# Kernel tuning notes

Measured on AMD Instinct MI355X. Metric: run time of the kernel, lower is better.

Reference implementation:

```python
import jax, jax.numpy as jnp
import numpy as np

N = 100000
E = 1600000
D = 128          # f_gru_in == f_gru_out
G = 128          # f_gather
K = 4            # n_etypes
STEPS = 3        # n_gconv_steps


def setup_inputs() -> dict:
    key = jax.random.key(0)
    ks = jax.random.split(key, 16)
    s = 0.05
    return {
        "features": jax.random.normal(ks[0], (N, D), jnp.float32),
        "src": jax.random.randint(ks[1], (E,), 0, N, jnp.int32),
        "dst": jax.random.randint(ks[2], (E,), 0, N, jnp.int32),
        "etypes": jax.random.randint(ks[3], (E,), 0, K, jnp.int32),
        # per-etype edge linears (torch Linear: y = x W^T + b)
        "W_et": jax.random.normal(ks[4], (K, D, D), jnp.float32) * s,
        "b_et": jax.random.normal(ks[5], (K, D), jnp.float32) * s,
        # GRUCell weights, torch gate order (r, z, n)
        "W_ih": jax.random.normal(ks[6], (3 * D, D), jnp.float32) * s,
        "b_ih": jax.random.normal(ks[7], (3 * D,), jnp.float32) * s,
        "W_hh": jax.random.normal(ks[8], (3 * D, D), jnp.float32) * s,
        "b_hh": jax.random.normal(ks[9], (3 * D,), jnp.float32) * s,
        # gated output head
        "i_w": jax.random.normal(ks[10], (G, D + D), jnp.float32) * s,
        "i_b": jax.random.normal(ks[11], (G,), jnp.float32) * s,
        "j_w": jax.random.normal(ks[12], (G, D), jnp.float32) * s,
        "j_b": jax.random.normal(ks[13], (G,), jnp.float32) * s,
    }


def _gru_cell(a, h, W_ih, b_ih, W_hh, b_hh):
    gi = a @ W_ih.T + b_ih          # [N, 3D]
    gh = h @ W_hh.T + b_hh          # [N, 3D]
    ir, iz, in_ = jnp.split(gi, 3, axis=1)
    hr, hz, hn = jnp.split(gh, 3, axis=1)
    r = jax.nn.sigmoid(ir + hr)
    z = jax.nn.sigmoid(iz + hz)
    n = jnp.tanh(in_ + r * hn)
    return (1.0 - z) * n + z * h


def reference(features, src, dst, etypes, W_et, b_et, W_ih, b_ih, W_hh, b_hh,
              i_w, i_b, j_w, j_b):
    n_nodes = features.shape[0]
    h = features  # in_feats == out_feats -> no zero padding needed
    for _ in range(STEPS):
        # transform all nodes by every etype linear: [K, N, D]
        t = jnp.einsum('nd,kod->kno', h, W_et) + b_et[:, None, :]
        # gather per-edge message by (etype, src) then scatter-add to dst
        msg = t[etypes, src]                                  # [E, D]
        a = jax.ops.segment_sum(msg, dst, num_segments=n_nodes)
        h = _gru_cell(a, h, W_ih, b_ih, W_hh, b_hh)
    # dropout p=0 (eval) -> identity; gated output head
    gate = jax.nn.sigmoid(jnp.concatenate([h, features], axis=1) @ i_w.T + i_b)
    return gate * (h @ j_w.T + j_b)
```

## Files before the change

### kernel.cpp

```cpp
#include <hip/hip_runtime.h>
#include <hip/hip_bf16.h>

typedef __bf16 bf16;
typedef __attribute__((ext_vector_type(8))) __bf16 bf16x8;
typedef __attribute__((ext_vector_type(4))) float f32x4;

union BP { unsigned u; bf16 b[2]; };

#define SB() __builtin_amdgcn_sched_barrier(0)

__device__ __forceinline__ void dma16(const void* g, void* l) {
  __builtin_amdgcn_global_load_lds(
      (const __attribute__((address_space(1))) unsigned*)g,
      (__attribute__((address_space(3))) unsigned*)l, 16, 0, 0);
}

__global__ __launch_bounds__(256) void fused_k(const bf16* __restrict__ big,
                                               bf16* __restrict__ hbp,
                                               const bf16* __restrict__ wb,
                                               int M)
{
  const int lane = threadIdx.x & 63;
  const int w    = threadIdx.x >> 6;
  const int quad = lane >> 4;
  const int lr   = lane & 15;
  const int mbase = blockIdx.x * 128 + w * 32;

  __shared__ __align__(16) bf16 lds[128 * 136];
  __shared__ __align__(16) bf16 wlds[2][4096];

  const bf16* wcat = wb;
  const bf16* blk  = wb + 69632;
  const bf16 *ih0 = blk,             *ih1 = blk + 16384, *ihn = blk + 2 * 16384;
  const bf16 *hh0 = blk + 3 * 16384, *hh1 = blk + 4 * 16384, *hhn = blk + 5 * 16384;
  const bf16 *bih = wb + 217088, *bhh = wb + 217472;

  long r0 = mbase + lr;      if (r0 >= M) r0 = M - 1;
  long r1 = mbase + 16 + lr; if (r1 >= M) r1 = M - 1;

  dma16(wcat + (size_t)(w * 2)     * 512 + (size_t)lane * 8, &wlds[0][(w * 2) * 512]);
  dma16(wcat + (size_t)(w * 2 + 1) * 512 + (size_t)lane * 8, &wlds[0][(w * 2 + 1) * 512]);
  bf16x8 Ab[2][2];
  Ab[0][0] = *(const bf16x8*)(big + r0 * 544 + quad * 8);
  Ab[0][1] = *(const bf16x8*)(big + r1 * 544 + quad * 8);

  f32x4 acc[2][8];
#pragma unroll
  for (int i = 0; i < 2; ++i)
#pragma unroll
    for (int j = 0; j < 8; ++j) acc[i][j] = (f32x4){0.f, 0.f, 0.f, 0.f};

#pragma unroll
  for (int kk = 0; kk < 17; ++kk) {
    const int cur = kk & 1;
    const int nxt = cur ^ 1;
    if (kk + 1 < 17) {
      const size_t gb = (size_t)(kk + 1) * 4096;
      dma16(wcat + gb + (size_t)(w * 2)     * 512 + (size_t)lane * 8, &wlds[nxt][(w * 2) * 512]);
      dma16(wcat + gb + (size_t)(w * 2 + 1) * 512 + (size_t)lane * 8, &wlds[nxt][(w * 2 + 1) * 512]);
      const int kc = (kk + 1) * 32 + quad * 8;
      Ab[nxt][0] = *(const bf16x8*)(big + r0 * 544 + kc);
      Ab[nxt][1] = *(const bf16x8*)(big + r1 * 544 + kc);
    }
    SB();
    if (kk + 1 < 17) asm volatile("s_waitcnt vmcnt(4)" ::: "memory");
    else             asm volatile("s_waitcnt vmcnt(0)" ::: "memory");
    SB();
    __builtin_amdgcn_s_barrier();
    SB();
    __builtin_amdgcn_s_setprio(1);
#pragma unroll
    for (int ct = 0; ct < 8; ++ct) {
      bf16x8 b = *(const bf16x8*)&wlds[cur][(ct * 64 + lane) * 8];
      acc[0][ct] = __builtin_amdgcn_mfma_f32_16x16x32_bf16(Ab[cur][0], b, acc[0][ct], 0, 0, 0);
      acc[1][ct] = __builtin_amdgcn_mfma_f32_16x16x32_bf16(Ab[cur][1], b, acc[1][ct], 0, 0, 0);
    }
    __builtin_amdgcn_s_setprio(0);
    SB();
    __builtin_amdgcn_s_barrier();
    SB();
  }

  const bf16* wptr0 = ih0; const bf16* wptr1 = hh0; const bf16* wptr2 = ih1;
  const bf16* wptr3 = hh1; const bf16* wptr4 = ihn; const bf16* wptr5 = hhn;
  {
    if (w == 0) { dma16(wptr0 + (size_t)lane * 8, &wlds[0][0 * 512]);
                  dma16(wptr4 + (size_t)lane * 8, &wlds[0][4 * 512]); }
    if (w == 1) { dma16(wptr1 + (size_t)lane * 8, &wlds[0][1 * 512]);
                  dma16(wptr5 + (size_t)lane * 8, &wlds[0][5 * 512]); }
    if (w == 2) { dma16(wptr2 + (size_t)lane * 8, &wlds[0][2 * 512]); }
    if (w == 3) { dma16(wptr3 + (size_t)lane * 8, &wlds[0][3 * 512]); }
  }

  bf16x8 hf[2][4];
#pragma unroll
  for (int kk = 0; kk < 4; ++kk) {
    hf[0][kk] = *(const bf16x8*)(hbp + r0 * 128 + kk * 32 + quad * 8);
    hf[1][kk] = *(const bf16x8*)(hbp + r1 * 128 + kk * 32 + quad * 8);
  }
#pragma unroll
  for (int ct = 0; ct < 8; ++ct) {
    const int nl = ct * 16 + lr;
#pragma unroll
    for (int rt = 0; rt < 2; ++rt) {
      const int rowb = w * 32 + rt * 16 + quad * 4;
#pragma unroll
      for (int r = 0; r < 4; ++r)
        lds[(rowb + r) * 136 + nl] = (bf16)acc[rt][ct][r];
    }
  }
  bf16x8 af[2][4];
#pragma unroll
  for (int kk = 0; kk < 4; ++kk) {
    af[0][kk] = *(const bf16x8*)(lds + (w * 32 + lr) * 136 + kk * 32 + quad * 8);
    af[1][kk] = *(const bf16x8*)(lds + (w * 32 + 16 + lr) * 136 + kk * 32 + quad * 8);
  }
#pragma unroll
  for (int kk = 0; kk < 4; ++kk) {
    *(bf16x8*)(lds + (w * 32 + lr) * 136 + kk * 32 + quad * 8)      = hf[0][kk];
    *(bf16x8*)(lds + (w * 32 + 16 + lr) * 136 + kk * 32 + quad * 8) = hf[1][kk];
  }
  __syncthreads();

#pragma unroll 1
  for (int ch = 0; ch < 8; ++ch) {
    f32x4 c[4][2];
#pragma unroll
    for (int s = 0; s < 4; ++s)
#pragma unroll
      for (int i = 0; i < 2; ++i) c[s][i] = (f32x4){0.f, 0.f, 0.f, 0.f};

#pragma unroll
    for (int kk = 0; kk < 4; ++kk) {
      const int cur = kk & 1;
      const int nx  = cur ^ 1;
      {
        size_t koff;
        if (kk < 3) koff = (size_t)((kk + 1) * 8 + ch) * 512;
        else        koff = (size_t)(ch < 7 ? ch + 1 : 7) * 512;
        if (w == 0) { dma16(wptr0 + koff + (size_t)lane * 8, &wlds[nx][0 * 512]);
                      dma16(wptr4 + koff + (size_t)lane * 8, &wlds[nx][4 * 512]); }
        if (w == 1) { dma16(wptr1 + koff + (size_t)lane * 8, &wlds[nx][1 * 512]);
                      dma16(wptr5 + koff + (size_t)lane * 8, &wlds[nx][5 * 512]); }
        if (w == 2) { dma16(wptr2 + koff + (size_t)lane * 8, &wlds[nx][2 * 512]); }
        if (w == 3) { dma16(wptr3 + koff + (size_t)lane * 8, &wlds[nx][3 * 512]); }
      }
      SB();
      if (w < 2) asm volatile("s_waitcnt vmcnt(2)" ::: "memory");
      else       asm volatile("s_waitcnt vmcnt(1)" ::: "memory");
      SB();
      __builtin_amdgcn_s_barrier();
      SB();
      bf16x8 g0 = *(const bf16x8*)&wlds[cur][(0 * 64 + lane) * 8];
      bf16x8 g1 = *(const bf16x8*)&wlds[cur][(1 * 64 + lane) * 8];
      bf16x8 g2 = *(const bf16x8*)&wlds[cur][(2 * 64 + lane) * 8];
      bf16x8 g3 = *(const bf16x8*)&wlds[cur][(3 * 64 + lane) * 8];
      bf16x8 g4 = *(const bf16x8*)&wlds[cur][(4 * 64 + lane) * 8];
      bf16x8 g5 = *(const bf16x8*)&wlds[cur][(5 * 64 + lane) * 8];
      __builtin_amdgcn_s_setprio(1);
      c[0][0] = __builtin_amdgcn_mfma_f32_16x16x32_bf16(af[0][kk], g0, c[0][0], 0, 0, 0);
      c[0][1] = __builtin_amdgcn_mfma_f32_16x16x32_bf16(af[1][kk], g0, c[0][1], 0, 0, 0);
      c[0][0] = __builtin_amdgcn_mfma_f32_16x16x32_bf16(hf[0][kk], g1, c[0][0], 0, 0, 0);
      c[0][1] = __builtin_amdgcn_mfma_f32_16x16x32_bf16(hf[1][kk], g1, c[0][1], 0, 0, 0);
      c[1][0] = __builtin_amdgcn_mfma_f32_16x16x32_bf16(af[0][kk], g2, c[1][0], 0, 0, 0);
      c[1][1] = __builtin_amdgcn_mfma_f32_16x16x32_bf16(af[1][kk], g2, c[1][1], 0, 0, 0);
      c[1][0] = __builtin_amdgcn_mfma_f32_16x16x32_bf16(hf[0][kk], g3, c[1][0], 0, 0, 0);
      c[1][1] = __builtin_amdgcn_mfma_f32_16x16x32_bf16(hf[1][kk], g3, c[1][1], 0, 0, 0);
      c[2][0] = __builtin_amdgcn_mfma_f32_16x16x32_bf16(af[0][kk], g4, c[2][0], 0, 0, 0);
      c[2][1] = __builtin_amdgcn_mfma_f32_16x16x32_bf16(af[1][kk], g4, c[2][1], 0, 0, 0);
      c[3][0] = __builtin_amdgcn_mfma_f32_16x16x32_bf16(hf[0][kk], g5, c[3][0], 0, 0, 0);
      c[3][1] = __builtin_amdgcn_mfma_f32_16x16x32_bf16(hf[1][kk], g5, c[3][1], 0, 0, 0);
      __builtin_amdgcn_s_setprio(0);

      if (kk == 3) {
        const int col = ch * 16 + lr;
        const float br = (float)bih[col]       + (float)bhh[col];
        const float bz = (float)bih[128 + col] + (float)bhh[128 + col];
        const float bi = (float)bih[256 + col];
        const float bh = (float)bhh[256 + col];
#pragma unroll
        for (int rt = 0; rt < 2; ++rt) {
          const int rowb = w * 32 + rt * 16 + quad * 4;
#pragma unroll
          for (int r = 0; r < 4; ++r) {
            const int li = (rowb + r) * 136 + col;
            const float hv = (float)lds[li];
            const float rr = 1.f / (1.f + __expf(-(c[0][rt][r] + br)));
            const float zz = 1.f / (1.f + __expf(-(c[1][rt][r] + bz)));
            const float xn = c[2][rt][r] + bi + rr * (c[3][rt][r] + bh);
            const float e2 = __expf(2.f * xn);
            const float nn = 1.f - 2.f / (e2 + 1.f);
            lds[li] = (bf16)((1.f - zz) * nn + zz * hv);
          }
        }
      }
      SB();
      __builtin_amdgcn_s_barrier();
      SB();
    }
  }

  __syncthreads();
  const int tr = threadIdx.x >> 4;
  const int tc = (threadIdx.x & 15) * 8;
#pragma unroll
  for (int i = 0; i < 8; ++i) {
    const int row = i * 16 + tr;
    const int grow = blockIdx.x * 128 + row;
    if (grow < M) {
      bf16x8 v = *(const bf16x8*)(lds + row * 136 + tc);
      *(bf16x8*)(hbp + (size_t)grow * 128 + tc) = v;
    }
  }
}

__global__ __launch_bounds__(256) void headf_k(const bf16* __restrict__ hbp,
                                               const void* __restrict__ featp,
                                               const bf16* __restrict__ wb,
                                               void* __restrict__ outp, int M,
                                               const int* __restrict__ flagp)
{
  const int lane = threadIdx.x & 63;
  const int w    = threadIdx.x >> 6;
  const int quad = lane >> 4;
  const int lr   = lane & 15;
  const int mbase = blockIdx.x * 128 + w * 32;

  __shared__ __align__(16) bf16 lds[128 * 136];
  __shared__ __align__(16) bf16 wlds[2][1536];

  const bf16* blk = wb + 69632;
  const bf16 *iwa = blk + 6 * 16384, *iwb = blk + 7 * 16384, *jw = blk + 8 * 16384;
  const bf16 *ib = wb + 217856, *jb = wb + 217984;
  const bool f32o = (*flagp != 0);

  long r0 = mbase + lr;      if (r0 >= M) r0 = M - 1;
  long r1 = mbase + 16 + lr; if (r1 >= M) r1 = M - 1;

  if (w == 0) dma16(iwa + (size_t)lane * 8, &wlds[0][0 * 512]);
  if (w == 1) dma16(iwb + (size_t)lane * 8, &wlds[0][1 * 512]);
  if (w == 2) dma16(jw  + (size_t)lane * 8, &wlds[0][2 * 512]);

  bf16x8 hf[2][4], ff[2][4];
#pragma unroll
  for (int kk = 0; kk < 4; ++kk) {
    hf[0][kk] = *(const bf16x8*)(hbp + r0 * 128 + kk * 32 + quad * 8);
    hf[1][kk] = *(const bf16x8*)(hbp + r1 * 128 + kk * 32 + quad * 8);
  }
  if (f32o) {
    const float* F = (const float*)featp;
#pragma unroll
    for (int kk = 0; kk < 4; ++kk) {
      const int kc = kk * 32 + quad * 8;
      f32x4 x0 = *(const f32x4*)(F + r0 * 128 + kc);
      f32x4 x1 = *(const f32x4*)(F + r0 * 128 + kc + 4);
      f32x4 y0 = *(const f32x4*)(F + r1 * 128 + kc);
      f32x4 y1 = *(const f32x4*)(F + r1 * 128 + kc + 4);
#pragma unroll
      for (int i = 0; i < 4; ++i) {
        ff[0][kk][i] = (bf16)x0[i]; ff[0][kk][i + 4] = (bf16)x1[i];
        ff[1][kk][i] = (bf16)y0[i]; ff[1][kk][i + 4] = (bf16)y1[i];
      }
    }
  } else {
    const bf16* F = (const bf16*)featp;
#pragma unroll
    for (int kk = 0; kk < 4; ++kk) {
      ff[0][kk] = *(const bf16x8*)(F + r0 * 128 + kk * 32 + quad * 8);
      ff[1][kk] = *(const bf16x8*)(F + r1 * 128 + kk * 32 + quad * 8);
    }
  }
  __syncthreads();

#pragma unroll 1
  for (int ch = 0; ch < 8; ++ch) {
    f32x4 cg[2], cu[2];
#pragma unroll
    for (int i = 0; i < 2; ++i) { cg[i] = (f32x4){0.f, 0.f, 0.f, 0.f};
                                  cu[i] = (f32x4){0.f, 0.f, 0.f, 0.f}; }
#pragma unroll
    for (int kk = 0; kk < 4; ++kk) {
      const int cur = kk & 1;
      const int nx  = cur ^ 1;
      {
        size_t koff;
        if (kk < 3) koff = (size_t)((kk + 1) * 8 + ch) * 512;
        else        koff = (size_t)(ch < 7 ? ch + 1 : 7) * 512;
        if (w == 0) dma16(iwa + koff + (size_t)lane * 8, &wlds[nx][0 * 512]);
        if (w == 1) dma16(iwb + koff + (size_t)lane * 8, &wlds[nx][1 * 512]);
        if (w == 2) dma16(jw  + koff + (size_t)lane * 8, &wlds[nx][2 * 512]);
      }
      SB();
      if (w < 3) asm volatile("s_waitcnt vmcnt(1)" ::: "memory");
      else       asm volatile("s_waitcnt vmcnt(0)" ::: "memory");
      SB();
      __builtin_amdgcn_s_barrier();
      SB();
      bf16x8 g0 = *(const bf16x8*)&wlds[cur][(0 * 64 + lane) * 8];
      bf16x8 g1 = *(const bf16x8*)&wlds[cur][(1 * 64 + lane) * 8];
      bf16x8 g2 = *(const bf16x8*)&wlds[cur][(2 * 64 + lane) * 8];
      __builtin_amdgcn_s_setprio(1);
      cg[0] = __builtin_amdgcn_mfma_f32_16x16x32_bf16(hf[0][kk], g0, cg[0], 0, 0, 0);
      cg[1] = __builtin_amdgcn_mfma_f32_16x16x32_bf16(hf[1][kk], g0, cg[1], 0, 0, 0);
      cg[0] = __builtin_amdgcn_mfma_f32_16x16x32_bf16(ff[0][kk], g1, cg[0], 0, 0, 0);
      cg[1] = __builtin_amdgcn_mfma_f32_16x16x32_bf16(ff[1][kk], g1, cg[1], 0, 0, 0);
      cu[0] = __builtin_amdgcn_mfma_f32_16x16x32_bf16(hf[0][kk], g2, cu[0], 0, 0, 0);
      cu[1] = __builtin_amdgcn_mfma_f32_16x16x32_bf16(hf[1][kk], g2, cu[1], 0, 0, 0);
      __builtin_amdgcn_s_setprio(0);

      if (kk == 3) {
        const int col = ch * 16 + lr;
        const float bg = (float)ib[col];
        const float bu = (float)jb[col];
#pragma unroll
        for (int rt = 0; rt < 2; ++rt) {
          const int rowb = w * 32 + rt * 16 + quad * 4;
#pragma unroll
          for (int r = 0; r < 4; ++r) {
            const float gl = cg[rt][r] + bg;
            const float uu = cu[rt][r] + bu;
            const float val = uu / (1.f + expf(-gl));
            if (f32o) {
              const int grow = blockIdx.x * 128 + rowb + r;
              if (grow < M)
                ((float*)outp)[(size_t)grow * 128 + col] = val;
            } else {
              lds[(rowb + r) * 136 + col] = (bf16)val;
            }
          }
        }
      }
      SB();
      __builtin_amdgcn_s_barrier();
      SB();
    }
  }

  __syncthreads();
  if (!f32o) {
    const int tr = threadIdx.x >> 4;
    const int tc = (threadIdx.x & 15) * 8;
#pragma unroll
    for (int i = 0; i < 8; ++i) {
      const int row = i * 16 + tr;
      const int grow = blockIdx.x * 128 + row;
      if (grow < M) {
        bf16x8 v = *(const bf16x8*)(lds + row * 136 + tc);
        *(bf16x8*)((bf16*)outp + (size_t)grow * 128 + tc) = v;
      }
    }
  }
}

__global__ __launch_bounds__(256) void detect_k(const unsigned short* __restrict__ f,
                                                int n16, int* __restrict__ flag)
{
  int i = blockIdx.x * 256 + threadIdx.x;
  int bad = 0;
  for (int j = i; j < n16; j += 256 * 1024) {
    int ex = (f[j] >> 7) & 0xFF;
    if (ex >= 0x87) bad = 1;
  }
  if (bad) atomicAdd(flag, 1);
}

__global__ __launch_bounds__(256) void feat_k(const void* __restrict__ src,
                                              bf16* __restrict__ hb, int n,
                                              const int* __restrict__ flag)
{
  int i = blockIdx.x * 256 + threadIdx.x;
  if (i >= n) return;
  if (*flag) hb[i] = (bf16)((const float*)src)[i];
  else       hb[i] = ((const bf16*)src)[i];
}

__global__ __launch_bounds__(256) void cvtw_k(
    const void* w_et, const void* b_et, const void* w_ih, const void* b_ih,
    const void* w_hh, const void* b_hh, const void* i_w, const void* i_b,
    const void* j_w, const void* j_b, bf16* __restrict__ wb,
    const int* __restrict__ flagp)
{
  int i = blockIdx.x * 256 + threadIdx.x;
  if (i >= 218112) return;
  const bool f32 = (*flagp != 0);
  auto rd = [&](const void* p, int idx) -> float {
    return f32 ? ((const float*)p)[idx] : (float)((const bf16*)p)[idx];
  };
  float v;
  if (i < 69632) {
    int e = i, j = e & 7, lane = (e >> 3) & 63, ct = (e >> 9) & 7, kk = e >> 12;
    int n = ct * 16 + (lane & 15), k = kk * 32 + (lane >> 4) * 8 + j;
    if (k < 512)      v = rd(w_et, (k >> 7) * 16384 + n * 128 + (k & 127));
    else if (k < 516) v = rd(b_et, (k - 512) * 128 + n);
    else              v = 0.f;
  } else if (i < 217088) {
    int blk = (i - 69632) >> 14, e = (i - 69632) & 16383;
    int j = e & 7, lane = (e >> 3) & 63, ct = (e >> 9) & 7, kk = e >> 12;
    int n = ct * 16 + (lane & 15), k = kk * 32 + (lane >> 4) * 8 + j;
    const void* src; int idx;
    switch (blk) {
      case 0: src = w_ih; idx = n * 128 + k; break;
      case 1: src = w_ih; idx = (128 + n) * 128 + k; break;
      case 2: src = w_ih; idx = (256 + n) * 128 + k; break;
      case 3: src = w_hh; idx = n * 128 + k; break;
      case 4: src = w_hh; idx = (128 + n) * 128 + k; break;
      case 5: src = w_hh; idx = (256 + n) * 128 + k; break;
      case 6: src = i_w;  idx = n * 256 + k; break;
      case 7: src = i_w;  idx = n * 256 + 128 + k; break;
      default: src = j_w; idx = n * 128 + k; break;
    }
    v = rd(src, idx);
  } else {
    int o = i - 217088;
    if (o < 384)      v = rd(b_ih, o);
    else if (o < 768) v = rd(b_hh, o - 384);
    else if (o < 896) v = rd(i_b, o - 768);
    else              v = rd(j_b, o - 896);
  }
  wb[i] = (bf16)v;
}

__global__ __launch_bounds__(256) void hist_k(const int* __restrict__ dst,
                                              const int* __restrict__ ety,
                                              int* __restrict__ deg, int E)
{
  int e = blockIdx.x * 256 + threadIdx.x;
  if (e < E) atomicAdd(&deg[dst[e] * 4 + ety[e]], 1);
}

__global__ __launch_bounds__(512) void scan1_k(const int* __restrict__ deg, int* __restrict__ rp,
                                               int* __restrict__ part, int n)
{
  __shared__ int buf[512];
  int i = blockIdx.x * 512 + threadIdx.x;
  int v = (i < n) ? deg[i] : 0;
  buf[threadIdx.x] = v;
  __syncthreads();
#pragma unroll
  for (int off = 1; off < 512; off <<= 1) {
    int t = 0;
    if (threadIdx.x >= off) t = buf[threadIdx.x - off];
    __syncthreads();
    buf[threadIdx.x] += t;
    __syncthreads();
  }
  if (i < n) rp[i] = buf[threadIdx.x] - v;
  if (threadIdx.x == 511) part[blockIdx.x] = buf[511];
}

__global__ __launch_bounds__(1024) void scan2_k(int* __restrict__ part, int nb, int* __restrict__ total)
{
  __shared__ int buf[1024];
  int t0 = threadIdx.x;
  int v = (t0 < nb) ? part[t0] : 0;
  buf[t0] = v;
  __syncthreads();
#pragma unroll
  for (int off = 1; off < 1024; off <<= 1) {
    int t = 0;
    if (t0 >= off) t = buf[t0 - off];
    __syncthreads();
    buf[t0] += t;
    __syncthreads();
  }
  if (t0 < nb) part[t0] = buf[t0] - v;
  if (t0 == 1023) *total = buf[1023];
}

__global__ __launch_bounds__(512) void scan3_k(int* __restrict__ rp, const int* __restrict__ part, int n)
{
  int i = blockIdx.x * 512 + threadIdx.x;
  if (i < n) rp[i] += part[blockIdx.x];
}

__global__ __launch_bounds__(256) void fill_k(const int* __restrict__ src, const int* __restrict__ dst,
                                              const int* __restrict__ ety, const int* __restrict__ rp,
                                              int* __restrict__ fil, int* __restrict__ bkt, int E)
{
  int e = blockIdx.x * 256 + threadIdx.x;
  if (e < E) {
    int key = dst[e] * 4 + ety[e];
    int pos = rp[key] + atomicAdd(&fil[key], 1);
    bkt[pos] = src[e];
  }
}

__global__ __launch_bounds__(256) void agg_k(const bf16* __restrict__ hb,
                                             const int* __restrict__ rp,
                                             const int* __restrict__ bkt,
                                             bf16* __restrict__ aggH, int N)
{
  const int lane = threadIdx.x & 63;
  const int n = blockIdx.x * 4 + (threadIdx.x >> 6);
  if (n >= N) return;
  const unsigned* hp = (const unsigned*)hb;
  unsigned* outp = (unsigned*)aggH + (size_t)n * 272;
  const int e0 = rp[n * 4];
  const int e1 = rp[n * 4 + 1];
  const int e2 = rp[n * 4 + 2];
  const int e3 = rp[n * 4 + 3];
  const int e4 = rp[n * 4 + 4];

  float t0 = 0.f, t1 = 0.f;
  float s10 = 0.f, s11 = 0.f;
  float s20 = 0.f, s21 = 0.f;
  float s30 = 0.f, s31 = 0.f;

  int base = e0;
  for (; base + 8 <= e4; base += 8) {
    unsigned u[8];
#pragma unroll
    for (int t = 0; t < 8; ++t)
      u[t] = hp[(unsigned)bkt[base + t] * 64u + (unsigned)lane];
#pragma unroll
    for (int t = 0; t < 8; ++t) {
      const int i = base + t;
      t0 += __uint_as_float(u[t] << 16);
      t1 += __uint_as_float(u[t] & 0xffff0000u);
      s10 = (i < e1) ? t0 : s10;  s11 = (i < e1) ? t1 : s11;
      s20 = (i < e2) ? t0 : s20;  s21 = (i < e2) ? t1 : s21;
      s30 = (i < e3) ? t0 : s30;  s31 = (i < e3) ? t1 : s31;
    }
  }
  if (base < e4) {
    const int last = e4 - 1;
    unsigned u[8];
#pragma unroll
    for (int t = 0; t < 8; ++t) {
      int i = base + t; i = i <= last ? i : last;
      u[t] = hp[(unsigned)bkt[i] * 64u + (unsigned)lane];
    }
#pragma unroll
    for (int t = 0; t < 8; ++t) {
      const int i = base + t;
      const bool ok = (i <= last);
      const float v0 = __uint_as_float(u[t] << 16);
      const float v1 = __uint_as_float(u[t] & 0xffff0000u);
      t0 += ok ? v0 : 0.f;
      t1 += ok ? v1 : 0.f;
      s10 = (i < e1) ? t0 : s10;  s11 = (i < e1) ? t1 : s11;
      s20 = (i < e2) ? t0 : s20;  s21 = (i < e2) ? t1 : s21;
      s30 = (i < e3) ? t0 : s30;  s31 = (i < e3) ? t1 : s31;
    }
  }

  BP o;
  o.b[0] = (bf16)s10;         o.b[1] = (bf16)s11;         outp[0 * 64 + lane] = o.u;
  o.b[0] = (bf16)(s20 - s10); o.b[1] = (bf16)(s21 - s11); outp[1 * 64 + lane] = o.u;
  o.b[0] = (bf16)(s30 - s20); o.b[1] = (bf16)(s31 - s21); outp[2 * 64 + lane] = o.u;
  o.b[0] = (bf16)(t0 - s30);  o.b[1] = (bf16)(t1 - s31);  outp[3 * 64 + lane] = o.u;
  if (lane < 16) {
    BP z; z.b[0] = (bf16)0.f; z.b[1] = (bf16)0.f;
    if (lane == 0) { z.b[0] = (bf16)(float)(e1 - e0); z.b[1] = (bf16)(float)(e2 - e1); }
    if (lane == 1) { z.b[0] = (bf16)(float)(e3 - e2); z.b[1] = (bf16)(float)(e4 - e3); }
    outp[256 + lane] = z.u;
  }
}

extern "C" void kernel_launch(void* const* d_in, const int* in_sizes, int n_in,
                              void* d_out, int out_size, void* d_ws, size_t ws_size,
                              hipStream_t stream)
{
  const void* feat = d_in[0];
  const int*  src  = (const int*)d_in[1];
  const int*  dst  = (const int*)d_in[2];
  const int*  ety  = (const int*)d_in[3];

  const int N = in_sizes[0] / 128;
  const int E = in_sizes[1];
  const int total = N * 128;

  char* p = (char*)d_ws;
  auto alloc = [&](size_t bytes) -> char* {
    char* q = p;
    p += (bytes + 255) & ~(size_t)255;
    return q;
  };
  bf16* big  = (bf16*)alloc((size_t)N * 544 * 2);
  bf16* hb   = (bf16*)alloc((size_t)total * 2);
  bf16* wb   = (bf16*)alloc(218112 * 2);
  int*  rp   = (int*) alloc(((size_t)4 * N + 1) * 4);
  int*  deg  = (int*) alloc((size_t)4 * N * 4);
  int*  bkt  = (int*) alloc((size_t)E * 4);
  int*  part = (int*) alloc(1024 * 4);
  int*  flag = (int*) alloc(64);

  const int gE  = (E + 255) / 256;
  const int gT  = (total + 255) / 256;
  const int gM  = (N + 127) / 128;
  const int n4  = 4 * N;
  const int gS  = (n4 + 511) / 512;

  hipMemsetAsync(flag, 0, 4, stream);
  detect_k<<<1024, 256, 0, stream>>>((const unsigned short*)feat, 2000000, flag);
  feat_k<<<gT, 256, 0, stream>>>(feat, hb, total, flag);
  cvtw_k<<<(218112 + 255) / 256, 256, 0, stream>>>(
      d_in[4], d_in[5], d_in[6], d_in[7], d_in[8],
      d_in[9], d_in[10], d_in[11], d_in[12], d_in[13], wb, flag);

  hipMemsetAsync(deg, 0, (size_t)n4 * 4, stream);
  hist_k<<<gE, 256, 0, stream>>>(dst, ety, deg, E);
  scan1_k<<<gS, 512, 0, stream>>>(deg, rp, part, n4);
  scan2_k<<<1, 1024, 0, stream>>>(part, gS, rp + n4);
  scan3_k<<<gS, 512, 0, stream>>>(rp, part, n4);
  hipMemsetAsync(deg, 0, (size_t)n4 * 4, stream);
  fill_k<<<gE, 256, 0, stream>>>(src, dst, ety, rp, deg, bkt, E);

  for (int step = 0; step < 3; ++step) {
    agg_k<<<(N + 3) / 4, 256, 0, stream>>>(hb, rp, bkt, big, N);
    fused_k<<<gM, 256, 0, stream>>>(big, hb, wb, N);
  }

  headf_k<<<gM, 256, 0, stream>>>(hb, feat, wb, d_out, N, flag);
}
```

Measured before the change: 842.5 us.

## Fuse neighbor aggregation into GRU kernel with ping-pong hidden state buffers

```diff
diff --git a/kernel.cpp b/kernel.cpp
--- a/kernel.cpp
+++ b/kernel.cpp
@@ -15,10 +15,13 @@
       (__attribute__((address_space(3))) unsigned*)l, 16, 0, 0);
 }
 
-__global__ __launch_bounds__(256) void fused_k(const bf16* __restrict__ big,
-                                               bf16* __restrict__ hbp,
-                                               const bf16* __restrict__ wb,
-                                               int M)
+__global__ __launch_bounds__(256) void fused2_k(bf16* __restrict__ big,
+                                                const bf16* hbin,
+                                                bf16* hbout,
+                                                const bf16* __restrict__ wb,
+                                                const int* __restrict__ rp,
+                                                const int* __restrict__ bkt,
+                                                int M, int do_gather)
 {
   const int lane = threadIdx.x & 63;
   const int w    = threadIdx.x >> 6;
@@ -28,6 +31,72 @@
 
   __shared__ __align__(16) bf16 lds[128 * 136];
   __shared__ __align__(16) bf16 wlds[2][4096];
+
+  if (do_gather) {
+    const unsigned* hp = (const unsigned*)hbin;
+#pragma unroll 1
+    for (int ii = 0; ii < 32; ++ii) {
+      const int n = blockIdx.x * 128 + w * 32 + ii;
+      if (n >= M) break;
+      unsigned* outp = (unsigned*)big + (size_t)n * 272;
+      const int e0 = rp[n * 4];
+      const int e1 = rp[n * 4 + 1];
+      const int e2 = rp[n * 4 + 2];
+      const int e3 = rp[n * 4 + 3];
+      const int e4 = rp[n * 4 + 4];
+      float t0 = 0.f, t1 = 0.f;
+      float s10 = 0.f, s11 = 0.f, s20 = 0.f, s21 = 0.f, s30 = 0.f, s31 = 0.f;
+      int base = e0;
+      for (; base + 8 <= e4; base += 8) {
+        unsigned u[8];
+#pragma unroll
+        for (int t = 0; t < 8; ++t)
+          u[t] = hp[(unsigned)bkt[base + t] * 64u + (unsigned)lane];
+#pragma unroll
+        for (int t = 0; t < 8; ++t) {
+          const int i = base + t;
+          t0 += __uint_as_float(u[t] << 16);
+          t1 += __uint_as_float(u[t] & 0xffff0000u);
+          s10 = (i < e1) ? t0 : s10;  s11 = (i < e1) ? t1 : s11;
+          s20 = (i < e2) ? t0 : s20;  s21 = (i < e2) ? t1 : s21;
+          s30 = (i < e3) ? t0 : s30;  s31 = (i < e3) ? t1 : s31;
+        }
+      }
+      if (base < e4) {
+        const int last = e4 - 1;
+        unsigned u[8];
+#pragma unroll
+        for (int t = 0; t < 8; ++t) {
+          int i = base + t; i = i <= last ? i : last;
+          u[t] = hp[(unsigned)bkt[i] * 64u + (unsigned)lane];
+        }
+#pragma unroll
+        for (int t = 0; t < 8; ++t) {
+          const int i = base + t;
+          const bool ok = (i <= last);
+          const float v0 = __uint_as_float(u[t] << 16);
+          const float v1 = __uint_as_float(u[t] & 0xffff0000u);
+          t0 += ok ? v0 : 0.f;
+          t1 += ok ? v1 : 0.f;
+          s10 = (i < e1) ? t0 : s10;  s11 = (i < e1) ? t1 : s11;
+          s20 = (i < e2) ? t0 : s20;  s21 = (i < e2) ? t1 : s21;
+          s30 = (i < e3) ? t0 : s30;  s31 = (i < e3) ? t1 : s31;
+        }
+      }
+      BP o;
+      o.b[0] = (bf16)s10;         o.b[1] = (bf16)s11;         outp[0 * 64 + lane] = o.u;
+      o.b[0] = (bf16)(s20 - s10); o.b[1] = (bf16)(s21 - s11); outp[1 * 64 + lane] = o.u;
+      o.b[0] = (bf16)(s30 - s20); o.b[1] = (bf16)(s31 - s21); outp[2 * 64 + lane] = o.u;
+      o.b[0] = (bf16)(t0 - s30);  o.b[1] = (bf16)(t1 - s31);  outp[3 * 64 + lane] = o.u;
+      if (lane < 16) {
+        BP z; z.b[0] = (bf16)0.f; z.b[1] = (bf16)0.f;
+        if (lane == 0) { z.b[0] = (bf16)(float)(e1 - e0); z.b[1] = (bf16)(float)(e2 - e1); }
+        if (lane == 1) { z.b[0] = (bf16)(float)(e3 - e2); z.b[1] = (bf16)(float)(e4 - e3); }
+        outp[256 + lane] = z.u;
+      }
+    }
+    __syncthreads();
+  }
 
   const bf16* wcat = wb;
   const bf16* blk  = wb + 69632;
@@ -95,8 +164,8 @@
   bf16x8 hf[2][4];
 #pragma unroll
   for (int kk = 0; kk < 4; ++kk) {
-    hf[0][kk] = *(const bf16x8*)(hbp + r0 * 128 + kk * 32 + quad * 8);
-    hf[1][kk] = *(const bf16x8*)(hbp + r1 * 128 + kk * 32 + quad * 8);
+    hf[0][kk] = *(const bf16x8*)(hbin + r0 * 128 + kk * 32 + quad * 8);
+    hf[1][kk] = *(const bf16x8*)(hbin + r1 * 128 + kk * 32 + quad * 8);
   }
 #pragma unroll
   for (int ct = 0; ct < 8; ++ct) {
@@ -209,7 +278,7 @@
     const int grow = blockIdx.x * 128 + row;
     if (grow < M) {
       bf16x8 v = *(const bf16x8*)(lds + row * 136 + tc);
-      *(bf16x8*)(hbp + (size_t)grow * 128 + tc) = v;
+      *(bf16x8*)(hbout + (size_t)grow * 128 + tc) = v;
     }
   }
 }
@@ -502,9 +571,7 @@
   const int e4 = rp[n * 4 + 4];
 
   float t0 = 0.f, t1 = 0.f;
-  float s10 = 0.f, s11 = 0.f;
-  float s20 = 0.f, s21 = 0.f;
-  float s30 = 0.f, s31 = 0.f;
+  float s10 = 0.f, s11 = 0.f, s20 = 0.f, s21 = 0.f, s30 = 0.f, s31 = 0.f;
 
   int base = e0;
   for (; base + 8 <= e4; base += 8) {
@@ -584,6 +651,9 @@
   int*  bkt  = (int*) alloc((size_t)E * 4);
   int*  part = (int*) alloc(1024 * 4);
   int*  flag = (int*) alloc(64);
+  size_t used = (size_t)(p - (char*)d_ws);
+  const bool pp = (used + (size_t)total * 2 <= ws_size);
+  bf16* hb1 = pp ? (bf16*)alloc((size_t)total * 2) : nullptr;
 
   const int gE  = (E + 255) / 256;
   const int gT  = (total + 255) / 256;
@@ -606,10 +676,21 @@
   hipMemsetAsync(deg, 0, (size_t)n4 * 4, stream);
   fill_k<<<gE, 256, 0, stream>>>(src, dst, ety, rp, deg, bkt, E);
 
-  for (int step = 0; step < 3; ++step) {
-    agg_k<<<(N + 3) / 4, 256, 0, stream>>>(hb, rp, bkt, big, N);
-    fused_k<<<gM, 256, 0, stream>>>(big, hb, wb, N);
-  }
-
-  headf_k<<<gM, 256, 0, stream>>>(hb, feat, wb, d_out, N, flag);
-}
+  const bf16* hfinal;
+  if (pp) {
+    bf16* hin = hb; bf16* hout = hb1;
+    for (int step = 0; step < 3; ++step) {
+      fused2_k<<<gM, 256, 0, stream>>>(big, hin, hout, wb, rp, bkt, N, 1);
+      bf16* t = hin; hin = hout; hout = t;
+    }
+    hfinal = hin;
+  } else {
+    for (int step = 0; step < 3; ++step) {
+      agg_k<<<(N + 3) / 4, 256, 0, stream>>>(hb, rp, bkt, big, N);
+      fused2_k<<<gM, 256, 0, stream>>>(big, hb, hb, wb, rp, bkt, N, 0);
+    }
+    hfinal = hb;
+  }
+
+  headf_k<<<gM, 256, 0, stream>>>(hfinal, feat, wb, d_out, N, flag);
+}
```

After: 1.113 ms. +32.1%, slower.
